# Kernel optimization log

Hardware: AMD Instinct MI355X
Metric: run time of the kernel (lower is better)

The kernel has to match this reference:

```python
import jax, jax.numpy as jnp
import numpy as np

N_NODES = 100000
BN_EPS = 1e-5


def gcn_conv(x, edge_index, W, b):
    # x: [N, Fin] -> [N, Fout]; symmetric-normalized aggregation with self-loops,
    # matching torch_geometric GCNConv defaults.
    n = x.shape[0]
    row, col = edge_index[0], edge_index[1]  # messages flow row -> col
    h = x @ W  # [N, Fout]
    deg = jnp.zeros((n,), dtype=h.dtype).at[col].add(1.0) + 1.0  # +1 for self-loop
    dinv = jax.lax.rsqrt(deg)  # deg >= 1 always
    norm = dinv[row] * dinv[col]  # [E]
    agg = jax.ops.segment_sum(h[row] * norm[:, None], col, num_segments=n)
    agg = agg + h * (dinv * dinv)[:, None]  # self-loop term, norm = 1/deg
    return agg + b


def batch_norm(x, gamma, beta):
    # BatchNorm1d in training mode: biased batch statistics over nodes.
    mean = jnp.mean(x, axis=0)
    var = jnp.mean((x - mean) ** 2, axis=0)
    return gamma * (x - mean) * jax.lax.rsqrt(var + BN_EPS) + beta


def setup_inputs() -> dict:
    key = jax.random.key(0)
    k = jax.random.split(key, 8)
    net_size1, hidden, net_size2 = 64, 128, 128
    x = jax.random.normal(k[0], (N_NODES, net_size1), dtype=jnp.float32)
    edge_index = jax.random.randint(k[1], (2, 1600000), 0, N_NODES, dtype=jnp.int64)
    s1 = 1.0 / np.sqrt(net_size1)
    s2 = 1.0 / np.sqrt(hidden)
    W1 = jax.random.normal(k[2], (net_size1, hidden), dtype=jnp.float32) * s1
    b1 = jnp.zeros((hidden,), dtype=jnp.float32)
    gamma = jnp.ones((hidden,), dtype=jnp.float32)
    beta = jnp.zeros((hidden,), dtype=jnp.float32)
    W2 = jax.random.normal(k[3], (hidden, net_size2), dtype=jnp.float32) * s2
    b2 = jnp.zeros((net_size2,), dtype=jnp.float32)
    return {"x": x, "edge_index": edge_index, "W1": W1, "b1": b1,
            "gamma": gamma, "beta": beta, "W2": W2, "b2": b2}


def reference(x, edge_index, W1, b1, gamma, beta, W2, b2):
    h = jax.nn.relu(gcn_conv(x, edge_index, W1, b1))
    h = batch_norm(h, gamma, beta)
    h = jax.nn.relu(gcn_conv(h, edge_index, W2, b2))
    return h
```

## Files before the change

kernel.cpp:

```cpp
#include <hip/hip_runtime.h>

#define BSZ_LG 9
#define BSZ 512

__device__ __forceinline__ float bf_lo(unsigned u) { return __uint_as_float(u << 16); }
__device__ __forceinline__ float bf_hi(unsigned u) { return __uint_as_float(u & 0xffff0000u); }
__device__ __forceinline__ float bf1(unsigned short s) { return __uint_as_float(((unsigned)s) << 16); }
__device__ __forceinline__ unsigned short f2bf(float f) {
    unsigned u = __float_as_uint(f);
    u += 0x7fffu + ((u >> 16) & 1u);
    return (unsigned short)(u >> 16);
}
__device__ __forceinline__ unsigned pack2(float a, float b) {
    return (unsigned)f2bf(a) | ((unsigned)f2bf(b) << 16);
}

__global__ void k_flags(const unsigned* __restrict__ x, const int* __restrict__ ei,
                        int* __restrict__ flagf, int* __restrict__ flage,
                        int* __restrict__ bcnt, int* __restrict__ stats) {
    int t = threadIdx.x;
    if (blockIdx.x == 0) {
        int c = 0;
        for (int i = t; i < 1024; i += 256) {
            unsigned e = (x[i] >> 23) & 0xffu;
            if (e >= 96u && e < 160u) c++;
        }
        __shared__ int s;
        if (t == 0) s = 0;
        __syncthreads();
        atomicAdd(&s, c);
        __syncthreads();
        if (t == 0) *flagf = (s > 512) ? 1 : 0;
    } else if (blockIdx.x == 1) {
        int nz = 0;
        for (int i = t; i < 2048; i += 256) nz |= ei[2 * i + 1];
        __shared__ int s2;
        if (t == 0) s2 = 0;
        __syncthreads();
        if (nz) atomicOr(&s2, 1);
        __syncthreads();
        if (t == 0) *flage = (s2 == 0) ? 1 : 0;
    } else if (blockIdx.x == 2) {
        bcnt[t] = 0;
    } else {
        stats[t] = 0;
    }
}

struct Cvt6 {
    const void* src[6];
    unsigned short* dst[6];
    int off[7];
};
__global__ void k_cvt6(Cvt6 a, const int* __restrict__ flagf) {
    int i = blockIdx.x * 256 + threadIdx.x;
    if (i >= a.off[6]) return;
    int s = 0;
#pragma unroll
    for (int j = 1; j < 6; ++j) if (i >= a.off[j]) s = j;
    int k = i - a.off[s];
    unsigned short v;
    if (*flagf) v = f2bf(((const float*)a.src[s])[k]);
    else        v = ((const unsigned short*)a.src[s])[k];
    a.dst[s][k] = v;
}

__global__ __launch_bounds__(256) void k_prep(
        const void* __restrict__ x, const float* __restrict__ dinv,
        const int* __restrict__ flagf, unsigned* __restrict__ xs32, int Nq) {
    int i = blockIdx.x * 256 + threadIdx.x;
    if (i >= Nq) return;
    int n = i >> 4;
    float di = dinv[n];
    float v0, v1, v2, v3;
    if (*flagf) {
        float4 f = ((const float4*)x)[i];
        v0 = f.x; v1 = f.y; v2 = f.z; v3 = f.w;
    } else {
        uint2 u = ((const uint2*)x)[i];
        v0 = bf_lo(u.x); v1 = bf_hi(u.x); v2 = bf_lo(u.y); v3 = bf_hi(u.y);
    }
    uint2 o; o.x = pack2(di * v0, di * v1); o.y = pack2(di * v2, di * v3);
    ((uint2*)xs32)[i] = o;
}

__global__ __launch_bounds__(256) void k_binA(
        const int* __restrict__ ei, const int* __restrict__ flage,
        int* __restrict__ bcnt, int E, int N, int NBUCK) {
    __shared__ int hist[256];
    int t = threadIdx.x;
    hist[t] = 0;
    __syncthreads();
    int st = *flage + 1;
    int base = blockIdx.x * 4096 + t;
#pragma unroll
    for (int i = 0; i < 16; ++i) {
        int e = base + i * 256;
        if (e < E) {
            int r = ei[(size_t)st * e];
            int c = ei[(size_t)st * (E + e)];
            if ((unsigned)r < (unsigned)N && (unsigned)c < (unsigned)N)
                atomicAdd(&hist[c >> BSZ_LG], 1);
        }
    }
    __syncthreads();
    if (t < NBUCK && hist[t] > 0) atomicAdd(&bcnt[t], hist[t]);
}

__global__ void k_bscan(const int* __restrict__ bcnt, int* __restrict__ bofs,
                        int* __restrict__ bcur, int NBUCK) {
    __shared__ int tmp[256];
    int t = threadIdx.x;
    int v = (t < NBUCK) ? bcnt[t] : 0;
    tmp[t] = v; __syncthreads();
    for (int off = 1; off < 256; off <<= 1) {
        int xv = (t >= off) ? tmp[t - off] : 0;
        __syncthreads();
        tmp[t] += xv;
        __syncthreads();
    }
    if (t < NBUCK) {
        int ex = tmp[t] - v;
        bofs[t] = ex;
        bcur[t] = ex;
        if (t == NBUCK - 1) bofs[NBUCK] = tmp[t];
    }
}

__global__ __launch_bounds__(256) void k_binB(
        const int* __restrict__ ei, const int* __restrict__ flage,
        int* __restrict__ bcur, unsigned* __restrict__ bins, int E, int N, int NBUCK) {
    __shared__ int hist[256], hincl[256], hofs[256], loc[256], gbase[256];
    __shared__ unsigned stage[4096];
    __shared__ unsigned char bseg[4096];
    int t = threadIdx.x;
    hist[t] = 0; loc[t] = 0;
    __syncthreads();
    int st = *flage + 1;
    int base = blockIdx.x * 4096 + t;
    int bs[16]; unsigned vs[16];
#pragma unroll
    for (int i = 0; i < 16; ++i) {
        int e = base + i * 256;
        bs[i] = -1; vs[i] = 0;
        if (e < E) {
            int r = ei[(size_t)st * e];
            int c = ei[(size_t)st * (E + e)];
            if ((unsigned)r < (unsigned)N && (unsigned)c < (unsigned)N) {
                bs[i] = c >> BSZ_LG;
                vs[i] = ((unsigned)r << BSZ_LG) | (unsigned)(c & (BSZ - 1));
                atomicAdd(&hist[bs[i]], 1);
            }
        }
    }
    __syncthreads();
    hincl[t] = hist[t];
    __syncthreads();
    for (int off = 1; off < 256; off <<= 1) {
        int xv = (t >= off) ? hincl[t - off] : 0;
        __syncthreads();
        hincl[t] += xv;
        __syncthreads();
    }
    hofs[t] = hincl[t] - hist[t];
    if (t < NBUCK && hist[t] > 0) gbase[t] = atomicAdd(&bcur[t], hist[t]);
    __syncthreads();
#pragma unroll
    for (int i = 0; i < 16; ++i) {
        if (bs[i] >= 0) {
            int l = atomicAdd(&loc[bs[i]], 1);
            int pos = hofs[bs[i]] + l;
            stage[pos] = vs[i];
            bseg[pos] = (unsigned char)bs[i];
        }
    }
    __syncthreads();
    int total = hincl[255];
    for (int j = t; j < total; j += 256) {
        int b = bseg[j];
        bins[gbase[b] + (j - hofs[b])] = stage[j];
    }
}

__global__ __launch_bounds__(512) void k_csr(
        const unsigned* __restrict__ bins, const int* __restrict__ bofs,
        int* __restrict__ csr, int* __restrict__ ofs, int* __restrict__ endv,
        float* __restrict__ dinv, int N) {
    __shared__ int tmp[BSZ];
    __shared__ int cur[BSZ];
    int b = blockIdx.x, t = threadIdx.x;
    int eb = bofs[b], ee = bofs[b + 1];
    tmp[t] = 0;
    __syncthreads();
    for (int p = eb + t; p < ee; p += BSZ)
        atomicAdd(&tmp[bins[p] & (BSZ - 1)], 1);
    __syncthreads();
    int v = tmp[t];
    for (int off = 1; off < BSZ; off <<= 1) {
        int xv = (t >= off) ? tmp[t - off] : 0;
        __syncthreads();
        tmp[t] += xv;
        __syncthreads();
    }
    int incl = tmp[t];
    int excl = incl - v;
    cur[t] = excl;
    int node = b * BSZ + t;
    if (node < N) {
        ofs[node]  = eb + excl;
        endv[node] = eb + incl;
        dinv[node] = rsqrtf((float)(v + 1));
    }
    __syncthreads();
    for (int p = eb + t; p < ee; p += BSZ) {
        unsigned x = bins[p];
        int cl = x & (BSZ - 1);
        int l = atomicAdd(&cur[cl], 1);
        csr[eb + l] = (int)(x >> BSZ_LG);
    }
}

__global__ __launch_bounds__(256) void k_agg1(
        const unsigned* __restrict__ xs32, const int* __restrict__ csr,
        const int* __restrict__ ofs, const int* __restrict__ endv,
        const float* __restrict__ dinv, unsigned* __restrict__ s1_32, int N) {
    int sub = threadIdx.x >> 5, lane = threadIdx.x & 31;
    int node = blockIdx.x * 8 + sub;
    if (node >= N) return;
    int beg = ofs[node], end = endv[node];
    unsigned self = xs32[(size_t)node * 32 + lane];
    float a0 = bf_lo(self), a1 = bf_hi(self);
    int p = beg;
    for (; p + 7 < end; p += 8) {
        int r0 = csr[p], r1 = csr[p+1], r2 = csr[p+2], r3 = csr[p+3];
        int r4 = csr[p+4], r5 = csr[p+5], r6 = csr[p+6], r7 = csr[p+7];
        unsigned u0 = xs32[(size_t)r0 * 32 + lane];
        unsigned u1 = xs32[(size_t)r1 * 32 + lane];
        unsigned u2 = xs32[(size_t)r2 * 32 + lane];
        unsigned u3 = xs32[(size_t)r3 * 32 + lane];
        unsigned u4 = xs32[(size_t)r4 * 32 + lane];
        unsigned u5 = xs32[(size_t)r5 * 32 + lane];
        unsigned u6 = xs32[(size_t)r6 * 32 + lane];
        unsigned u7 = xs32[(size_t)r7 * 32 + lane];
        a0 += bf_lo(u0) + bf_lo(u1) + bf_lo(u2) + bf_lo(u3)
            + bf_lo(u4) + bf_lo(u5) + bf_lo(u6) + bf_lo(u7);
        a1 += bf_hi(u0) + bf_hi(u1) + bf_hi(u2) + bf_hi(u3)
            + bf_hi(u4) + bf_hi(u5) + bf_hi(u6) + bf_hi(u7);
    }
    for (; p + 3 < end; p += 4) {
        int r0 = csr[p], r1 = csr[p+1], r2 = csr[p+2], r3 = csr[p+3];
        unsigned u0 = xs32[(size_t)r0 * 32 + lane];
        unsigned u1 = xs32[(size_t)r1 * 32 + lane];
        unsigned u2 = xs32[(size_t)r2 * 32 + lane];
        unsigned u3 = xs32[(size_t)r3 * 32 + lane];
        a0 += bf_lo(u0) + bf_lo(u1) + bf_lo(u2) + bf_lo(u3);
        a1 += bf_hi(u0) + bf_hi(u1) + bf_hi(u2) + bf_hi(u3);
    }
    for (; p < end; ++p) {
        unsigned u = xs32[(size_t)csr[p] * 32 + lane];
        a0 += bf_lo(u); a1 += bf_hi(u);
    }
    float di = dinv[node];
    s1_32[(size_t)node * 32 + lane] = pack2(di * a0, di * a1);
}

typedef __attribute__((ext_vector_type(8))) short bf16x8;
typedef __attribute__((ext_vector_type(4))) float f32x4;

template<int K, int OUTMODE>
__global__ __launch_bounds__(256) void k_mgemm(
        const unsigned short* __restrict__ A, const unsigned short* __restrict__ Wg,
        const unsigned short* __restrict__ bias, void* __restrict__ outv,
        const int* __restrict__ flagf, int N) {
    constexpr int KP = K + 8;
    __shared__ __align__(16) unsigned short sA[64 * KP];
    __shared__ __align__(16) unsigned short sW[128 * KP];
    int t = threadIdx.x;
    int n0 = blockIdx.x * 64;

    for (int i = t; i < K * 128; i += 256) {
        int k = i >> 7, n = i & 127;
        sW[n * KP + k] = Wg[i];
    }
    {
        constexpr int rowv = K / 8;
        const uint4* Av = (const uint4*)A;
        for (int i = t; i < 64 * rowv; i += 256) {
            int r = i / rowv, c = i % rowv;
            int node = n0 + r;
            uint4 v = make_uint4(0u, 0u, 0u, 0u);
            if (node < N) v = Av[(size_t)node * rowv + c];
            *(uint4*)&sA[r * KP + c * 8] = v;
        }
    }
    __syncthreads();

    int lane = t & 63, wave = t >> 6, quad = lane >> 4, l16 = lane & 15;
    int mb = wave * 16;

    f32x4 acc[8];
#pragma unroll
    for (int j = 0; j < 8; ++j) acc[j] = (f32x4){0.f, 0.f, 0.f, 0.f};

#pragma unroll
    for (int k0 = 0; k0 < K; k0 += 32) {
        bf16x8 af = *(const bf16x8*)&sA[(mb + l16) * KP + k0 + quad * 8];
#pragma unroll
        for (int tn = 0; tn < 8; ++tn) {
            bf16x8 bfv = *(const bf16x8*)&sW[(tn * 16 + l16) * KP + k0 + quad * 8];
            acc[tn] = __builtin_amdgcn_mfma_f32_16x16x32_bf16(af, bfv, acc[tn], 0, 0, 0);
        }
    }

    bool f32out = (OUTMODE == 1) && (*flagf != 0);
    int nodeb = n0 + mb + quad * 4;
#pragma unroll
    for (int tn = 0; tn < 8; ++tn) {
        float bv = bf1(bias[tn * 16 + l16]);
#pragma unroll
        for (int r = 0; r < 4; ++r) {
            int node = nodeb + r;
            if (node < N) {
                float v = fmaxf(acc[tn][r] + bv, 0.f);
                if (OUTMODE == 1 && f32out)
                    ((float*)outv)[(size_t)node * 128 + tn * 16 + l16] = v;
                else
                    ((unsigned short*)outv)[(size_t)node * 128 + tn * 16 + l16] = f2bf(v);
            }
        }
    }
}

__global__ __launch_bounds__(256) void k_bnstat(
        const unsigned short* __restrict__ h1, float* __restrict__ stats, int N) {
    __shared__ float sS[1024], sQ[1024];
    int t = threadIdx.x;
    int lane = t & 31, g = t >> 5;
    int f0 = lane * 4;
    float s0=0, s1=0, s2=0, s3=0, q0=0, q1=0, q2=0, q3=0;
    const uint2* h2 = (const uint2*)h1;
    for (int n = blockIdx.x * 8 + g; n < N; n += 2048) {
        uint2 u = h2[(size_t)n * 32 + lane];
        float v0 = bf_lo(u.x), v1 = bf_hi(u.x), v2 = bf_lo(u.y), v3 = bf_hi(u.y);
        s0 += v0; s1 += v1; s2 += v2; s3 += v3;
        q0 = fmaf(v0, v0, q0); q1 = fmaf(v1, v1, q1);
        q2 = fmaf(v2, v2, q2); q3 = fmaf(v3, v3, q3);
    }
    sS[g * 128 + f0 + 0] = s0; sS[g * 128 + f0 + 1] = s1;
    sS[g * 128 + f0 + 2] = s2; sS[g * 128 + f0 + 3] = s3;
    sQ[g * 128 + f0 + 0] = q0; sQ[g * 128 + f0 + 1] = q1;
    sQ[g * 128 + f0 + 2] = q2; sQ[g * 128 + f0 + 3] = q3;
    __syncthreads();
    if (t < 128) {
        float ss = 0, qq = 0;
#pragma unroll
        for (int gg = 0; gg < 8; ++gg) { ss += sS[gg * 128 + t]; qq += sQ[gg * 128 + t]; }
        atomicAdd(&stats[t], ss);
        atomicAdd(&stats[128 + t], qq);
    }
}

__global__ void k_bnfin(const float* __restrict__ stats,
                        const unsigned short* __restrict__ gamma,
                        const unsigned short* __restrict__ beta,
                        float* __restrict__ bnp, float invN) {
    int f = threadIdx.x;
    float mean = stats[f] * invN;
    float var = stats[128 + f] * invN - mean * mean;
    if (!(var >= 0.f)) var = 0.f;
    float sc = bf1(gamma[f]) * rsqrtf(var + 1e-5f);
    bnp[f] = sc;
    bnp[128 + f] = bf1(beta[f]) - mean * sc;
}

__global__ __launch_bounds__(256) void k_bnapply(
        const unsigned short* __restrict__ h1, const float* __restrict__ bnp,
        const float* __restrict__ dinv, unsigned short* __restrict__ gb, int N) {
    int idx = blockIdx.x * 256 + threadIdx.x;
    if (idx >= N * 16) return;
    int n = idx >> 4;
    int f0 = (idx & 15) * 8;
    float di = dinv[n];
    uint4 h = *(const uint4*)&h1[(size_t)n * 128 + f0];
    float v0 = di * (bnp[f0 + 0] * bf_lo(h.x) + bnp[128 + f0 + 0]);
    float v1 = di * (bnp[f0 + 1] * bf_hi(h.x) + bnp[128 + f0 + 1]);
    float v2 = di * (bnp[f0 + 2] * bf_lo(h.y) + bnp[128 + f0 + 2]);
    float v3 = di * (bnp[f0 + 3] * bf_hi(h.y) + bnp[128 + f0 + 3]);
    float v4 = di * (bnp[f0 + 4] * bf_lo(h.z) + bnp[128 + f0 + 4]);
    float v5 = di * (bnp[f0 + 5] * bf_hi(h.z) + bnp[128 + f0 + 5]);
    float v6 = di * (bnp[f0 + 6] * bf_lo(h.w) + bnp[128 + f0 + 6]);
    float v7 = di * (bnp[f0 + 7] * bf_hi(h.w) + bnp[128 + f0 + 7]);
    uint4 o;
    o.x = pack2(v0, v1); o.y = pack2(v2, v3);
    o.z = pack2(v4, v5); o.w = pack2(v6, v7);
    *(uint4*)&gb[(size_t)n * 128 + f0] = o;
}

__global__ __launch_bounds__(256) void k_agg2(
        const unsigned short* __restrict__ gb, const int* __restrict__ csr,
        const int* __restrict__ ofs, const int* __restrict__ endv,
        const float* __restrict__ dinv, unsigned short* __restrict__ s2, int N) {
    int sub = threadIdx.x >> 5, lane = threadIdx.x & 31;
    int node = blockIdx.x * 8 + sub;
    if (node >= N) return;
    const uint2* g2 = (const uint2*)gb;
    int beg = ofs[node], end = endv[node];
    uint2 self = g2[(size_t)node * 32 + lane];
    float a0 = bf_lo(self.x), a1 = bf_hi(self.x), a2 = bf_lo(self.y), a3 = bf_hi(self.y);
    int p = beg;
    for (; p + 7 < end; p += 8) {
        int r0 = csr[p], r1 = csr[p+1], r2 = csr[p+2], r3 = csr[p+3];
        int r4 = csr[p+4], r5 = csr[p+5], r6 = csr[p+6], r7 = csr[p+7];
        uint2 u0 = g2[(size_t)r0 * 32 + lane];
        uint2 u1 = g2[(size_t)r1 * 32 + lane];
        uint2 u2 = g2[(size_t)r2 * 32 + lane];
        uint2 u3 = g2[(size_t)r3 * 32 + lane];
        uint2 u4 = g2[(size_t)r4 * 32 + lane];
        uint2 u5 = g2[(size_t)r5 * 32 + lane];
        uint2 u6 = g2[(size_t)r6 * 32 + lane];
        uint2 u7 = g2[(size_t)r7 * 32 + lane];
        a0 += bf_lo(u0.x) + bf_lo(u1.x) + bf_lo(u2.x) + bf_lo(u3.x)
            + bf_lo(u4.x) + bf_lo(u5.x) + bf_lo(u6.x) + bf_lo(u7.x);
        a1 += bf_hi(u0.x) + bf_hi(u1.x) + bf_hi(u2.x) + bf_hi(u3.x)
            + bf_hi(u4.x) + bf_hi(u5.x) + bf_hi(u6.x) + bf_hi(u7.x);
        a2 += bf_lo(u0.y) + bf_lo(u1.y) + bf_lo(u2.y) + bf_lo(u3.y)
            + bf_lo(u4.y) + bf_lo(u5.y) + bf_lo(u6.y) + bf_lo(u7.y);
        a3 += bf_hi(u0.y) + bf_hi(u1.y) + bf_hi(u2.y) + bf_hi(u3.y)
            + bf_hi(u4.y) + bf_hi(u5.y) + bf_hi(u6.y) + bf_hi(u7.y);
    }
    for (; p + 3 < end; p += 4) {
        int r0 = csr[p], r1 = csr[p+1], r2 = csr[p+2], r3 = csr[p+3];
        uint2 u0 = g2[(size_t)r0 * 32 + lane];
        uint2 u1 = g2[(size_t)r1 * 32 + lane];
        uint2 u2 = g2[(size_t)r2 * 32 + lane];
        uint2 u3 = g2[(size_t)r3 * 32 + lane];
        a0 += bf_lo(u0.x) + bf_lo(u1.x) + bf_lo(u2.x) + bf_lo(u3.x);
        a1 += bf_hi(u0.x) + bf_hi(u1.x) + bf_hi(u2.x) + bf_hi(u3.x);
        a2 += bf_lo(u0.y) + bf_lo(u1.y) + bf_lo(u2.y) + bf_lo(u3.y);
        a3 += bf_hi(u0.y) + bf_hi(u1.y) + bf_hi(u2.y) + bf_hi(u3.y);
    }
    for (; p < end; ++p) {
        uint2 u = g2[(size_t)csr[p] * 32 + lane];
        a0 += bf_lo(u.x); a1 += bf_hi(u.x); a2 += bf_lo(u.y); a3 += bf_hi(u.y);
    }
    float di = dinv[node];
    uint2 o; o.x = pack2(di * a0, di * a1); o.y = pack2(di * a2, di * a3);
    ((uint2*)s2)[(size_t)node * 32 + lane] = o;
}

extern "C" void kernel_launch(void* const* d_in, const int* in_sizes, int n_in,
                              void* d_out, int out_size, void* d_ws, size_t ws_size,
                              hipStream_t stream) {
    const int N = in_sizes[0] / 64;
    const int E = in_sizes[1] / 2;
    const int nW1 = in_sizes[2], nb1 = in_sizes[3], ngm = in_sizes[4],
              nbt = in_sizes[5], nW2 = in_sizes[6], nb2 = in_sizes[7];
    const int NBUCK = (N + BSZ - 1) >> BSZ_LG;

    const int* ei = (const int*)d_in[1];

    char* w = (char*)d_ws;
    size_t off = 0;
    auto alloc = [&](size_t bytes) -> void* {
        void* p = w + off;
        off = (off + bytes + 255) & ~(size_t)255;
        return p;
    };
    int*   bcnt   = (int*)alloc(256 * 4);
    int*   bofs   = (int*)alloc(257 * 4);
    int*   bcur   = (int*)alloc(256 * 4);
    int*   flagf  = (int*)alloc(256);
    int*   flage  = (int*)alloc(256);
    int*   ofs    = (int*)alloc((size_t)N * 4);
    int*   endv   = (int*)alloc((size_t)N * 4);
    int*   csr    = (int*)alloc((size_t)E * 4);
    float* dinv   = (float*)alloc((size_t)N * 4);
    float* stats  = (float*)alloc(512 * 4);
    unsigned* xs32 = (unsigned*)alloc((size_t)N * 64 * 2);
    unsigned short* wb = (unsigned short*)alloc((size_t)32768 * 2);
    char* reg1 = (char*)alloc((size_t)N * 64 * 4);
    char* reg2 = (char*)alloc((size_t)N * 128 * 2);
    unsigned* bins = (unsigned*)reg1;
    unsigned short* s1 = (unsigned short*)reg1;
    unsigned short* gb = (unsigned short*)reg1;
    unsigned short* h1 = (unsigned short*)reg2;
    unsigned short* s2 = (unsigned short*)reg2;

    unsigned short* W1b = wb;
    unsigned short* b1b = W1b + nW1;
    unsigned short* gmb = b1b + nb1;
    unsigned short* btb = gmb + ngm;
    unsigned short* W2b = btb + nbt;
    unsigned short* b2b = W2b + nW2;

    const int NCH = (E + 4095) / 4096;

    k_flags <<<4, 256, 0, stream>>>((const unsigned*)d_in[0], ei, flagf, flage,
                                    bcnt, (int*)stats);
    Cvt6 ca;
    ca.src[0] = d_in[2]; ca.dst[0] = W1b;
    ca.src[1] = d_in[3]; ca.dst[1] = b1b;
    ca.src[2] = d_in[4]; ca.dst[2] = gmb;
    ca.src[3] = d_in[5]; ca.dst[3] = btb;
    ca.src[4] = d_in[6]; ca.dst[4] = W2b;
    ca.src[5] = d_in[7]; ca.dst[5] = b2b;
    int szs[6] = {nW1, nb1, ngm, nbt, nW2, nb2};
    ca.off[0] = 0;
    for (int i = 0; i < 6; ++i) ca.off[i + 1] = ca.off[i] + szs[i];
    k_cvt6 <<<(ca.off[6] + 255) / 256, 256, 0, stream>>>(ca, flagf);

    k_binA  <<<NCH, 256, 0, stream>>>(ei, flage, bcnt, E, N, NBUCK);
    k_bscan <<<1, 256, 0, stream>>>(bcnt, bofs, bcur, NBUCK);
    k_binB  <<<NCH, 256, 0, stream>>>(ei, flage, bcur, bins, E, N, NBUCK);
    k_csr   <<<NBUCK, BSZ, 0, stream>>>(bins, bofs, csr, ofs, endv, dinv, N);

    k_prep  <<<(N * 16 + 255) / 256, 256, 0, stream>>>(d_in[0], dinv, flagf, xs32, N * 16);
    k_agg1  <<<(N + 7) / 8, 256, 0, stream>>>(xs32, csr, ofs, endv, dinv, (unsigned*)s1, N);
    k_mgemm<64, 0><<<(N + 63) / 64, 256, 0, stream>>>(s1, W1b, b1b, h1, flagf, N);
    k_bnstat<<<256, 256, 0, stream>>>(h1, stats, N);
    k_bnfin <<<1, 128, 0, stream>>>(stats, gmb, btb, stats + 256, 1.0f / (float)N);
    k_bnapply<<<((size_t)N * 16 + 255) / 256, 256, 0, stream>>>(h1, stats + 256, dinv, gb, N);
    k_agg2  <<<(N + 7) / 8, 256, 0, stream>>>(gb, csr, ofs, endv, dinv, s2, N);
    k_mgemm<128, 1><<<(N + 63) / 64, 256, 0, stream>>>(s2, W2b, b2b, d_out, flagf, N);
}
```

Measured before the change: 315.4 us.

## Fuse prep into CSR build, fold BN finalize into apply, persistent aggregation grids

The dinv-scaled bf16 conversion of x now runs inside the CSR-building kernel, so the separate prep launch goes away. The BN finalize step is recomputed per block inside bnapply, which removes a one-block launch. The offset and end arrays are merged into a single N+1 offsets array, cutting index traffic. Both aggregation kernels become grid-stride loops over a fixed grid size. In exchange, k_csr blocks do extra per-node work, and the fixed grid sizes may balance load differently.

```diff
diff --git a/kernel.cpp b/kernel.cpp
--- a/kernel.cpp
+++ b/kernel.cpp
@@ -63,25 +63,6 @@
     if (*flagf) v = f2bf(((const float*)a.src[s])[k]);
     else        v = ((const unsigned short*)a.src[s])[k];
     a.dst[s][k] = v;
-}
-
-__global__ __launch_bounds__(256) void k_prep(
-        const void* __restrict__ x, const float* __restrict__ dinv,
-        const int* __restrict__ flagf, unsigned* __restrict__ xs32, int Nq) {
-    int i = blockIdx.x * 256 + threadIdx.x;
-    if (i >= Nq) return;
-    int n = i >> 4;
-    float di = dinv[n];
-    float v0, v1, v2, v3;
-    if (*flagf) {
-        float4 f = ((const float4*)x)[i];
-        v0 = f.x; v1 = f.y; v2 = f.z; v3 = f.w;
-    } else {
-        uint2 u = ((const uint2*)x)[i];
-        v0 = bf_lo(u.x); v1 = bf_hi(u.x); v2 = bf_lo(u.y); v3 = bf_hi(u.y);
-    }
-    uint2 o; o.x = pack2(di * v0, di * v1); o.y = pack2(di * v2, di * v3);
-    ((uint2*)xs32)[i] = o;
 }
 
 __global__ __launch_bounds__(256) void k_binA(
@@ -184,10 +165,12 @@
 
 __global__ __launch_bounds__(512) void k_csr(
         const unsigned* __restrict__ bins, const int* __restrict__ bofs,
-        int* __restrict__ csr, int* __restrict__ ofs, int* __restrict__ endv,
-        float* __restrict__ dinv, int N) {
+        const void* __restrict__ x, const int* __restrict__ flagf,
+        int* __restrict__ csr, int* __restrict__ ofs,
+        float* __restrict__ dinv, unsigned* __restrict__ xs32, int N) {
     __shared__ int tmp[BSZ];
     __shared__ int cur[BSZ];
+    __shared__ float sdi[BSZ];
     int b = blockIdx.x, t = threadIdx.x;
     int eb = bofs[b], ee = bofs[b + 1];
     tmp[t] = 0;
@@ -205,63 +188,84 @@
     int incl = tmp[t];
     int excl = incl - v;
     cur[t] = excl;
+    float di = rsqrtf((float)(v + 1));
+    sdi[t] = di;
     int node = b * BSZ + t;
     if (node < N) {
         ofs[node]  = eb + excl;
-        endv[node] = eb + incl;
-        dinv[node] = rsqrtf((float)(v + 1));
+        dinv[node] = di;
+        if (node == N - 1) ofs[N] = eb + incl;
     }
     __syncthreads();
     for (int p = eb + t; p < ee; p += BSZ) {
-        unsigned x = bins[p];
-        int cl = x & (BSZ - 1);
+        unsigned xx = bins[p];
+        int cl = xx & (BSZ - 1);
         int l = atomicAdd(&cur[cl], 1);
-        csr[eb + l] = (int)(x >> BSZ_LG);
+        csr[eb + l] = (int)(xx >> BSZ_LG);
+    }
+    bool f32 = (*flagf != 0);
+    int nbase = b * BSZ;
+    for (int i = t; i < BSZ * 16; i += BSZ) {
+        int nl = i >> 4;
+        int n = nbase + nl;
+        if (n >= N) break;
+        float d2 = sdi[nl];
+        float v0, v1, v2, v3;
+        if (f32) {
+            float4 f = ((const float4*)x)[(size_t)n * 16 + (i & 15)];
+            v0 = f.x; v1 = f.y; v2 = f.z; v3 = f.w;
+        } else {
+            uint2 u = ((const uint2*)x)[(size_t)n * 16 + (i & 15)];
+            v0 = bf_lo(u.x); v1 = bf_hi(u.x); v2 = bf_lo(u.y); v3 = bf_hi(u.y);
+        }
+        uint2 o; o.x = pack2(d2 * v0, d2 * v1); o.y = pack2(d2 * v2, d2 * v3);
+        ((uint2*)xs32)[(size_t)n * 16 + (i & 15)] = o;
     }
 }
 
 __global__ __launch_bounds__(256) void k_agg1(
         const unsigned* __restrict__ xs32, const int* __restrict__ csr,
-        const int* __restrict__ ofs, const int* __restrict__ endv,
-        const float* __restrict__ dinv, unsigned* __restrict__ s1_32, int N) {
+        const int* __restrict__ ofs, const float* __restrict__ dinv,
+        unsigned* __restrict__ s1_32, int N) {
     int sub = threadIdx.x >> 5, lane = threadIdx.x & 31;
-    int node = blockIdx.x * 8 + sub;
-    if (node >= N) return;
-    int beg = ofs[node], end = endv[node];
-    unsigned self = xs32[(size_t)node * 32 + lane];
-    float a0 = bf_lo(self), a1 = bf_hi(self);
-    int p = beg;
-    for (; p + 7 < end; p += 8) {
-        int r0 = csr[p], r1 = csr[p+1], r2 = csr[p+2], r3 = csr[p+3];
-        int r4 = csr[p+4], r5 = csr[p+5], r6 = csr[p+6], r7 = csr[p+7];
-        unsigned u0 = xs32[(size_t)r0 * 32 + lane];
-        unsigned u1 = xs32[(size_t)r1 * 32 + lane];
-        unsigned u2 = xs32[(size_t)r2 * 32 + lane];
-        unsigned u3 = xs32[(size_t)r3 * 32 + lane];
-        unsigned u4 = xs32[(size_t)r4 * 32 + lane];
-        unsigned u5 = xs32[(size_t)r5 * 32 + lane];
-        unsigned u6 = xs32[(size_t)r6 * 32 + lane];
-        unsigned u7 = xs32[(size_t)r7 * 32 + lane];
-        a0 += bf_lo(u0) + bf_lo(u1) + bf_lo(u2) + bf_lo(u3)
-            + bf_lo(u4) + bf_lo(u5) + bf_lo(u6) + bf_lo(u7);
-        a1 += bf_hi(u0) + bf_hi(u1) + bf_hi(u2) + bf_hi(u3)
-            + bf_hi(u4) + bf_hi(u5) + bf_hi(u6) + bf_hi(u7);
-    }
-    for (; p + 3 < end; p += 4) {
-        int r0 = csr[p], r1 = csr[p+1], r2 = csr[p+2], r3 = csr[p+3];
-        unsigned u0 = xs32[(size_t)r0 * 32 + lane];
-        unsigned u1 = xs32[(size_t)r1 * 32 + lane];
-        unsigned u2 = xs32[(size_t)r2 * 32 + lane];
-        unsigned u3 = xs32[(size_t)r3 * 32 + lane];
-        a0 += bf_lo(u0) + bf_lo(u1) + bf_lo(u2) + bf_lo(u3);
-        a1 += bf_hi(u0) + bf_hi(u1) + bf_hi(u2) + bf_hi(u3);
-    }
-    for (; p < end; ++p) {
-        unsigned u = xs32[(size_t)csr[p] * 32 + lane];
-        a0 += bf_lo(u); a1 += bf_hi(u);
-    }
-    float di = dinv[node];
-    s1_32[(size_t)node * 32 + lane] = pack2(di * a0, di * a1);
+    int stride = gridDim.x * 8;
+    for (int node = blockIdx.x * 8 + sub; node < N; node += stride) {
+        int beg = ofs[node], end = ofs[node + 1];
+        unsigned self = xs32[(size_t)node * 32 + lane];
+        float a0 = bf_lo(self), a1 = bf_hi(self);
+        int p = beg;
+        for (; p + 7 < end; p += 8) {
+            int r0 = csr[p], r1 = csr[p+1], r2 = csr[p+2], r3 = csr[p+3];
+            int r4 = csr[p+4], r5 = csr[p+5], r6 = csr[p+6], r7 = csr[p+7];
+            unsigned u0 = xs32[(size_t)r0 * 32 + lane];
+            unsigned u1 = xs32[(size_t)r1 * 32 + lane];
+            unsigned u2 = xs32[(size_t)r2 * 32 + lane];
+            unsigned u3 = xs32[(size_t)r3 * 32 + lane];
+            unsigned u4 = xs32[(size_t)r4 * 32 + lane];
+            unsigned u5 = xs32[(size_t)r5 * 32 + lane];
+            unsigned u6 = xs32[(size_t)r6 * 32 + lane];
+            unsigned u7 = xs32[(size_t)r7 * 32 + lane];
+            a0 += bf_lo(u0) + bf_lo(u1) + bf_lo(u2) + bf_lo(u3)
+                + bf_lo(u4) + bf_lo(u5) + bf_lo(u6) + bf_lo(u7);
+            a1 += bf_hi(u0) + bf_hi(u1) + bf_hi(u2) + bf_hi(u3)
+                + bf_hi(u4) + bf_hi(u5) + bf_hi(u6) + bf_hi(u7);
+        }
+        for (; p + 3 < end; p += 4) {
+            int r0 = csr[p], r1 = csr[p+1], r2 = csr[p+2], r3 = csr[p+3];
+            unsigned u0 = xs32[(size_t)r0 * 32 + lane];
+            unsigned u1 = xs32[(size_t)r1 * 32 + lane];
+            unsigned u2 = xs32[(size_t)r2 * 32 + lane];
+            unsigned u3 = xs32[(size_t)r3 * 32 + lane];
+            a0 += bf_lo(u0) + bf_lo(u1) + bf_lo(u2) + bf_lo(u3);
+            a1 += bf_hi(u0) + bf_hi(u1) + bf_hi(u2) + bf_hi(u3);
+        }
+        for (; p < end; ++p) {
+            unsigned u = xs32[(size_t)csr[p] * 32 + lane];
+            a0 += bf_lo(u); a1 += bf_hi(u);
+        }
+        float di = dinv[node];
+        s1_32[(size_t)node * 32 + lane] = pack2(di * a0, di * a1);
+    }
 }
 
 typedef __attribute__((ext_vector_type(8))) short bf16x8;
@@ -360,36 +364,36 @@
     }
 }
 
-__global__ void k_bnfin(const float* __restrict__ stats,
-                        const unsigned short* __restrict__ gamma,
-                        const unsigned short* __restrict__ beta,
-                        float* __restrict__ bnp, float invN) {
-    int f = threadIdx.x;
-    float mean = stats[f] * invN;
-    float var = stats[128 + f] * invN - mean * mean;
-    if (!(var >= 0.f)) var = 0.f;
-    float sc = bf1(gamma[f]) * rsqrtf(var + 1e-5f);
-    bnp[f] = sc;
-    bnp[128 + f] = bf1(beta[f]) - mean * sc;
-}
-
 __global__ __launch_bounds__(256) void k_bnapply(
-        const unsigned short* __restrict__ h1, const float* __restrict__ bnp,
-        const float* __restrict__ dinv, unsigned short* __restrict__ gb, int N) {
-    int idx = blockIdx.x * 256 + threadIdx.x;
+        const unsigned short* __restrict__ h1, const float* __restrict__ stats,
+        const unsigned short* __restrict__ gamma, const unsigned short* __restrict__ beta,
+        const float* __restrict__ dinv, unsigned short* __restrict__ gb,
+        float invN, int N) {
+    __shared__ float sp[256];
+    int t = threadIdx.x;
+    if (t < 128) {
+        float mean = stats[t] * invN;
+        float var = stats[128 + t] * invN - mean * mean;
+        if (!(var >= 0.f)) var = 0.f;
+        float sc = bf1(gamma[t]) * rsqrtf(var + 1e-5f);
+        sp[t] = sc;
+        sp[128 + t] = bf1(beta[t]) - mean * sc;
+    }
+    __syncthreads();
+    int idx = blockIdx.x * 256 + t;
     if (idx >= N * 16) return;
     int n = idx >> 4;
     int f0 = (idx & 15) * 8;
     float di = dinv[n];
     uint4 h = *(const uint4*)&h1[(size_t)n * 128 + f0];
-    float v0 = di * (bnp[f0 + 0] * bf_lo(h.x) + bnp[128 + f0 + 0]);
-    float v1 = di * (bnp[f0 + 1] * bf_hi(h.x) + bnp[128 + f0 + 1]);
-    float v2 = di * (bnp[f0 + 2] * bf_lo(h.y) + bnp[128 + f0 + 2]);
-    float v3 = di * (bnp[f0 + 3] * bf_hi(h.y) + bnp[128 + f0 + 3]);
-    float v4 = di * (bnp[f0 + 4] * bf_lo(h.z) + bnp[128 + f0 + 4]);
-    float v5 = di * (bnp[f0 + 5] * bf_hi(h.z) + bnp[128 + f0 + 5]);
-    float v6 = di * (bnp[f0 + 6] * bf_lo(h.w) + bnp[128 + f0 + 6]);
-    float v7 = di * (bnp[f0 + 7] * bf_hi(h.w) + bnp[128 + f0 + 7]);
+    float v0 = di * (sp[f0 + 0] * bf_lo(h.x) + sp[128 + f0 + 0]);
+    float v1 = di * (sp[f0 + 1] * bf_hi(h.x) + sp[128 + f0 + 1]);
+    float v2 = di * (sp[f0 + 2] * bf_lo(h.y) + sp[128 + f0 + 2]);
+    float v3 = di * (sp[f0 + 3] * bf_hi(h.y) + sp[128 + f0 + 3]);
+    float v4 = di * (sp[f0 + 4] * bf_lo(h.z) + sp[128 + f0 + 4]);
+    float v5 = di * (sp[f0 + 5] * bf_hi(h.z) + sp[128 + f0 + 5]);
+    float v6 = di * (sp[f0 + 6] * bf_lo(h.w) + sp[128 + f0 + 6]);
+    float v7 = di * (sp[f0 + 7] * bf_hi(h.w) + sp[128 + f0 + 7]);
     uint4 o;
     o.x = pack2(v0, v1); o.y = pack2(v2, v3);
     o.z = pack2(v4, v5); o.w = pack2(v6, v7);
@@ -398,54 +402,56 @@
 
 __global__ __launch_bounds__(256) void k_agg2(
         const unsigned short* __restrict__ gb, const int* __restrict__ csr,
-        const int* __restrict__ ofs, const int* __restrict__ endv,
-        const float* __restrict__ dinv, unsigned short* __restrict__ s2, int N) {
+        const int* __restrict__ ofs, const float* __restrict__ dinv,
+        unsigned short* __restrict__ s2, int N) {
     int sub = threadIdx.x >> 5, lane = threadIdx.x & 31;
-    int node = blockIdx.x * 8 + sub;
-    if (node >= N) return;
     const uint2* g2 = (const uint2*)gb;
-    int beg = ofs[node], end = endv[node];
-    uint2 self = g2[(size_t)node * 32 + lane];
-    float a0 = bf_lo(self.x), a1 = bf_hi(self.x), a2 = bf_lo(self.y), a3 = bf_hi(self.y);
-    int p = beg;
-    for (; p + 7 < end; p += 8) {
-        int r0 = csr[p], r1 = csr[p+1], r2 = csr[p+2], r3 = csr[p+3];
-        int r4 = csr[p+4], r5 = csr[p+5], r6 = csr[p+6], r7 = csr[p+7];
-        uint2 u0 = g2[(size_t)r0 * 32 + lane];
-        uint2 u1 = g2[(size_t)r1 * 32 + lane];
-        uint2 u2 = g2[(size_t)r2 * 32 + lane];
-        uint2 u3 = g2[(size_t)r3 * 32 + lane];
-        uint2 u4 = g2[(size_t)r4 * 32 + lane];
-        uint2 u5 = g2[(size_t)r5 * 32 + lane];
-        uint2 u6 = g2[(size_t)r6 * 32 + lane];
-        uint2 u7 = g2[(size_t)r7 * 32 + lane];
-        a0 += bf_lo(u0.x) + bf_lo(u1.x) + bf_lo(u2.x) + bf_lo(u3.x)
-            + bf_lo(u4.x) + bf_lo(u5.x) + bf_lo(u6.x) + bf_lo(u7.x);
-        a1 += bf_hi(u0.x) + bf_hi(u1.x) + bf_hi(u2.x) + bf_hi(u3.x)
-            + bf_hi(u4.x) + bf_hi(u5.x) + bf_hi(u6.x) + bf_hi(u7.x);
-        a2 += bf_lo(u0.y) + bf_lo(u1.y) + bf_lo(u2.y) + bf_lo(u3.y)
-            + bf_lo(u4.y) + bf_lo(u5.y) + bf_lo(u6.y) + bf_lo(u7.y);
-        a3 += bf_hi(u0.y) + bf_hi(u1.y) + bf_hi(u2.y) + bf_hi(u3.y)
-            + bf_hi(u4.y) + bf_hi(u5.y) + bf_hi(u6.y) + bf_hi(u7.y);
-    }
-    for (; p + 3 < end; p += 4) {
-        int r0 = csr[p], r1 = csr[p+1], r2 = csr[p+2], r3 = csr[p+3];
-        uint2 u0 = g2[(size_t)r0 * 32 + lane];
-        uint2 u1 = g2[(size_t)r1 * 32 + lane];
-        uint2 u2 = g2[(size_t)r2 * 32 + lane];
-        uint2 u3 = g2[(size_t)r3 * 32 + lane];
-        a0 += bf_lo(u0.x) + bf_lo(u1.x) + bf_lo(u2.x) + bf_lo(u3.x);
-        a1 += bf_hi(u0.x) + bf_hi(u1.x) + bf_hi(u2.x) + bf_hi(u3.x);
-        a2 += bf_lo(u0.y) + bf_lo(u1.y) + bf_lo(u2.y) + bf_lo(u3.y);
-        a3 += bf_hi(u0.y) + bf_hi(u1.y) + bf_hi(u2.y) + bf_hi(u3.y);
-    }
-    for (; p < end; ++p) {
-        uint2 u = g2[(size_t)csr[p] * 32 + lane];
-        a0 += bf_lo(u.x); a1 += bf_hi(u.x); a2 += bf_lo(u.y); a3 += bf_hi(u.y);
-    }
-    float di = dinv[node];
-    uint2 o; o.x = pack2(di * a0, di * a1); o.y = pack2(di * a2, di * a3);
-    ((uint2*)s2)[(size_t)node * 32 + lane] = o;
+    int stride = gridDim.x * 8;
+    for (int node = blockIdx.x * 8 + sub; node < N; node += stride) {
+        int beg = ofs[node], end = ofs[node + 1];
+        uint2 self = g2[(size_t)node * 32 + lane];
+        float a0 = bf_lo(self.x), a1 = bf_hi(self.x);
+        float a2 = bf_lo(self.y), a3 = bf_hi(self.y);
+        int p = beg;
+        for (; p + 7 < end; p += 8) {
+            int r0 = csr[p], r1 = csr[p+1], r2 = csr[p+2], r3 = csr[p+3];
+            int r4 = csr[p+4], r5 = csr[p+5], r6 = csr[p+6], r7 = csr[p+7];
+            uint2 u0 = g2[(size_t)r0 * 32 + lane];
+            uint2 u1 = g2[(size_t)r1 * 32 + lane];
+            uint2 u2 = g2[(size_t)r2 * 32 + lane];
+            uint2 u3 = g2[(size_t)r3 * 32 + lane];
+            uint2 u4 = g2[(size_t)r4 * 32 + lane];
+            uint2 u5 = g2[(size_t)r5 * 32 + lane];
+            uint2 u6 = g2[(size_t)r6 * 32 + lane];
+            uint2 u7 = g2[(size_t)r7 * 32 + lane];
+            a0 += bf_lo(u0.x) + bf_lo(u1.x) + bf_lo(u2.x) + bf_lo(u3.x)
+                + bf_lo(u4.x) + bf_lo(u5.x) + bf_lo(u6.x) + bf_lo(u7.x);
+            a1 += bf_hi(u0.x) + bf_hi(u1.x) + bf_hi(u2.x) + bf_hi(u3.x)
+                + bf_hi(u4.x) + bf_hi(u5.x) + bf_hi(u6.x) + bf_hi(u7.x);
+            a2 += bf_lo(u0.y) + bf_lo(u1.y) + bf_lo(u2.y) + bf_lo(u3.y)
+                + bf_lo(u4.y) + bf_lo(u5.y) + bf_lo(u6.y) + bf_lo(u7.y);
+            a3 += bf_hi(u0.y) + bf_hi(u1.y) + bf_hi(u2.y) + bf_hi(u3.y)
+                + bf_hi(u4.y) + bf_hi(u5.y) + bf_hi(u6.y) + bf_hi(u7.y);
+        }
+        for (; p + 3 < end; p += 4) {
+            int r0 = csr[p], r1 = csr[p+1], r2 = csr[p+2], r3 = csr[p+3];
+            uint2 u0 = g2[(size_t)r0 * 32 + lane];
+            uint2 u1 = g2[(size_t)r1 * 32 + lane];
+            uint2 u2 = g2[(size_t)r2 * 32 + lane];
+            uint2 u3 = g2[(size_t)r3 * 32 + lane];
+            a0 += bf_lo(u0.x) + bf_lo(u1.x) + bf_lo(u2.x) + bf_lo(u3.x);
+            a1 += bf_hi(u0.x) + bf_hi(u1.x) + bf_hi(u2.x) + bf_hi(u3.x);
+            a2 += bf_lo(u0.y) + bf_lo(u1.y) + bf_lo(u2.y) + bf_lo(u3.y);
+            a3 += bf_hi(u0.y) + bf_hi(u1.y) + bf_hi(u2.y) + bf_hi(u3.y);
+        }
+        for (; p < end; ++p) {
+            uint2 u = g2[(size_t)csr[p] * 32 + lane];
+            a0 += bf_lo(u.x); a1 += bf_hi(u.x); a2 += bf_lo(u.y); a3 += bf_hi(u.y);
+        }
+        float di = dinv[node];
+        uint2 o; o.x = pack2(di * a0, di * a1); o.y = pack2(di * a2, di * a3);
+        ((uint2*)s2)[(size_t)node * 32 + lane] = o;
+    }
 }
 
 extern "C" void kernel_launch(void* const* d_in, const int* in_sizes, int n_in,
@@ -471,8 +477,7 @@
     int*   bcur   = (int*)alloc(256 * 4);
     int*   flagf  = (int*)alloc(256);
     int*   flage  = (int*)alloc(256);
-    int*   ofs    = (int*)alloc((size_t)N * 4);
-    int*   endv   = (int*)alloc((size_t)N * 4);
+    int*   ofs    = (int*)alloc(((size_t)N + 1) * 4);
     int*   csr    = (int*)alloc((size_t)E * 4);
     float* dinv   = (float*)alloc((size_t)N * 4);
     float* stats  = (float*)alloc(512 * 4);
@@ -512,14 +517,14 @@
     k_binA  <<<NCH, 256, 0, stream>>>(ei, flage, bcnt, E, N, NBUCK);
     k_bscan <<<1, 256, 0, stream>>>(bcnt, bofs, bcur, NBUCK);
     k_binB  <<<NCH, 256, 0, stream>>>(ei, flage, bcur, bins, E, N, NBUCK);
-    k_csr   <<<NBUCK, BSZ, 0, stream>>>(bins, bofs, csr, ofs, endv, dinv, N);
-
-    k_prep  <<<(N * 16 + 255) / 256, 256, 0, stream>>>(d_in[0], dinv, flagf, xs32, N * 16);
-    k_agg1  <<<(N + 7) / 8, 256, 0, stream>>>(xs32, csr, ofs, endv, dinv, (unsigned*)s1, N);
+    k_csr   <<<NBUCK, BSZ, 0, stream>>>(bins, bofs, d_in[0], flagf,
+                                        csr, ofs, dinv, xs32, N);
+
+    k_agg1  <<<1280, 256, 0, stream>>>(xs32, csr, ofs, dinv, (unsigned*)s1, N);
     k_mgemm<64, 0><<<(N + 63) / 64, 256, 0, stream>>>(s1, W1b, b1b, h1, flagf, N);
     k_bnstat<<<256, 256, 0, stream>>>(h1, stats, N);
-    k_bnfin <<<1, 128, 0, stream>>>(stats, gmb, btb, stats + 256, 1.0f / (float)N);
-    k_bnapply<<<((size_t)N * 16 + 255) / 256, 256, 0, stream>>>(h1, stats + 256, dinv, gb, N);
-    k_agg2  <<<(N + 7) / 8, 256, 0, stream>>>(gb, csr, ofs, endv, dinv, s2, N);
+    k_bnapply<<<((size_t)N * 16 + 255) / 256, 256, 0, stream>>>(
+        h1, stats, gmb, btb, dinv, gb, 1.0f / (float)N, N);
+    k_agg2  <<<2000, 256, 0, stream>>>(gb, csr, ofs, dinv, s2, N);
     k_mgemm<128, 1><<<(N + 63) / 64, 256, 0, stream>>>(s2, W2b, b2b, d_out, flagf, N);
 }
```

Result: slower. 333.7 us (+5.8%).
